# Kernel optimization log

Hardware: AMD Instinct MI355X
Metric: run time of the kernel (lower is better)

## Reference

```python
import jax, jax.numpy as jnp
import numpy as np

B, H, W, DIM = 8, 64, 64, 256
HEADS, DH = 8, 64
HID = HEADS * DH  # 512
EPS = 1e-5


def setup_inputs() -> dict:
    key = jax.random.key(0)
    k0, k1, k2 = jax.random.split(key, 3)
    return {
        "x": jax.random.normal(k0, (B, H, W, DIM), dtype=jnp.float32),
        "w_qkv": jax.random.normal(k1, (DIM, 3 * HID), dtype=jnp.float32) / np.sqrt(DIM),
        "gn_scale": jnp.ones((HID,), jnp.float32),
        "gn_bias": jnp.zeros((HID,), jnp.float32),
        "w_out": jax.random.normal(k2, (HID, DIM), dtype=jnp.float32) / np.sqrt(HID),
        "b_out": jnp.zeros((DIM,), jnp.float32),
    }


def reference(x, w_qkv, gn_scale, gn_bias, w_out, b_out):
    b, h, w, c = x.shape
    n = h * w
    scale = DH ** -0.5
    # 1x1 conv (no bias) == channel matmul
    qkv = jnp.einsum('bxyc,cf->bxyf', x, w_qkv)
    q, k, v = jnp.split(qkv, 3, axis=-1)
    # 'b x y (h c) -> b h c (x y)'
    to_heads = lambda t: t.reshape(b, n, HEADS, DH).transpose(0, 2, 3, 1)
    q, k, v = map(to_heads, (q, k, v))  # [b, heads, d, n]
    q = jax.nn.softmax(q, axis=-2) * scale  # softmax over feature dim d
    k = jax.nn.softmax(k, axis=-1)          # softmax over token dim n
    context = jnp.einsum('bhdn,bhen->bhde', k, v)   # small d x e context
    out = jnp.einsum('bhde,bhdn->bhen', context, q)  # [b, heads, e, n]
    # 'b h c (x y) -> b x y (h c)'
    out = out.transpose(0, 3, 1, 2).reshape(b, h, w, HID)
    # GroupNorm with 1 group: normalize over (H, W, C) per sample
    mu = out.mean(axis=(1, 2, 3), keepdims=True)
    var = out.var(axis=(1, 2, 3), keepdims=True)
    out = (out - mu) * jax.lax.rsqrt(var + EPS) * gn_scale + gn_bias
    # final 1x1 conv with bias
    return jnp.einsum('bxyf,fc->bxyc', out, w_out) + b_out
```

## Files before the change

### kernel.cpp

```cpp
#include <hip/hip_runtime.h>


typedef unsigned short ushort_t;
typedef __attribute__((ext_vector_type(8))) short short8;
typedef __attribute__((ext_vector_type(4))) float floatx4;

__device__ __forceinline__ float b2f(ushort_t u) {
  unsigned int i = ((unsigned int)u) << 16;
  float f;
  __builtin_memcpy(&f, &i, 4);
  return f;
}
__device__ __forceinline__ ushort_t f2b(float f) {
  unsigned int i;
  __builtin_memcpy(&i, &f, 4);
  unsigned int r = (i + 0x7FFFu + ((i >> 16) & 1u)) >> 16;
  return (ushort_t)r;
}

__device__ __forceinline__ void load_lds16(const ushort_t* g, ushort_t* l) {
  __builtin_amdgcn_global_load_lds(
      (const __attribute__((address_space(1))) unsigned int*)g,
      (__attribute__((address_space(3))) unsigned int*)l, 16, 0, 0);
}

__global__ __launch_bounds__(256) void cast_f32_bf16(
    const float* __restrict__ in, ushort_t* __restrict__ out) {
  long i = ((long)blockIdx.x * 256 + threadIdx.x) * 4;
  float4 v = *(const float4*)(in + i);
  ushort4 o;
  o.x = f2b(v.x);
  o.y = f2b(v.y);
  o.z = f2b(v.z);
  o.w = f2b(v.w);
  *(ushort4*)(out + i) = o;
}

__global__ __launch_bounds__(256) void transpose_f32_bf16(
    const float* __restrict__ in, ushort_t* __restrict__ out, int R, int C,
    const float* __restrict__ scale) {
  __shared__ ushort_t t[32][33];
  int c0 = blockIdx.x * 32, r0 = blockIdx.y * 32;
  int tx = threadIdx.x & 31, ty = threadIdx.x >> 5;
  for (int i = 0; i < 32; i += 8) {
    float s = scale ? scale[r0 + ty + i] : 1.0f;
    t[ty + i][tx] = f2b(in[(long)(r0 + ty + i) * C + c0 + tx] * s);
  }
  __syncthreads();
  for (int i = 0; i < 32; i += 8)
    out[(long)(c0 + ty + i) * R + r0 + tx] = t[tx][ty + i];
}

__global__ __launch_bounds__(64) void prep_gw_kernel(
    const float* __restrict__ gn_scale, const float* __restrict__ gn_bias,
    const float* __restrict__ w_out, const float* __restrict__ b_out,
    float* __restrict__ gw1, float* __restrict__ bias2) {
  int c = blockIdx.x * 64 + threadIdx.x;
  float g1 = 0.f, b2 = 0.f;
  for (int f = 0; f < 512; ++f) {
    float w = w_out[f * 256 + c];
    g1 += gn_scale[f] * w;
    b2 += gn_bias[f] * w;
  }
  gw1[c] = g1;
  bias2[c] = b2 + b_out[c];
}

template <int MODE, bool SWAP>
__global__ __launch_bounds__(256) void gemm_tpl(
    const ushort_t* __restrict__ A, const ushort_t* __restrict__ Bt,
    void* __restrict__ Cv, int M, int K, int F,
    const float* __restrict__ murs, const float* __restrict__ gw1,
    const float* __restrict__ bias2) {
  __shared__ __align__(16) ushort_t As[128][32];
  __shared__ __align__(16) ushort_t Bs[128][32];
  int tid = threadIdx.x;
  long m0 = (long)(SWAP ? blockIdx.y : blockIdx.x) * 128;
  long f0 = (long)(SWAP ? blockIdx.x : blockIdx.y) * 128;
  int wv = tid >> 6, lane = tid & 63;
  int wm = wv & 1, wf = wv >> 1;
  int l15 = lane & 15, quad = lane >> 4;

  floatx4 acc[4][4];
  floatx4 zero = {0.f, 0.f, 0.f, 0.f};
  for (int i = 0; i < 4; i++)
    for (int j = 0; j < 4; j++) acc[i][j] = zero;

  for (int k0 = 0; k0 < K; k0 += 32) {
    __syncthreads();
#pragma unroll
    for (int r = 0; r < 2; ++r) {
      int chunk = r * 256 + tid;
      int row = chunk >> 2;
      int kc = chunk & 3;
      load_lds16(A + (m0 + row) * (long)K + k0 + kc * 8, &As[row][kc * 8]);
      load_lds16(Bt + (f0 + row) * (long)K + k0 + kc * 8, &Bs[row][kc * 8]);
    }
    __syncthreads();
    short8 af[4], bfr[4];
#pragma unroll
    for (int mt = 0; mt < 4; mt++)
      af[mt] = *(const short8*)(&As[wm * 64 + mt * 16 + l15][quad * 8]);
#pragma unroll
    for (int ft = 0; ft < 4; ft++)
      bfr[ft] = *(const short8*)(&Bs[wf * 64 + ft * 16 + l15][quad * 8]);
#pragma unroll
    for (int mt = 0; mt < 4; mt++)
#pragma unroll
      for (int ft = 0; ft < 4; ft++)
        acc[mt][ft] = __builtin_amdgcn_mfma_f32_16x16x32_bf16(
            af[mt], bfr[ft], acc[mt][ft], 0, 0, 0);
  }

  {
    float* C = (float*)Cv;
    int b = (int)(m0 >> 12);
    float mu = murs[b * 2], rs = murs[b * 2 + 1];
#pragma unroll
    for (int mt = 0; mt < 4; mt++)
#pragma unroll
      for (int ft = 0; ft < 4; ft++) {
        long col = f0 + wf * 64 + ft * 16 + l15;
        float c1 = bias2[col] - rs * mu * gw1[col];
#pragma unroll
        for (int r = 0; r < 4; r++) {
          long row = m0 + wm * 64 + mt * 16 + quad * 4 + r;
          C[row * F + col] = rs * acc[mt][ft][r] + c1;
        }
      }
  }
}

__global__ __launch_bounds__(256) void kvctx_kernel(
    const ushort_t* __restrict__ xb, const ushort_t* __restrict__ wqkvT,
    float* __restrict__ ctxP, float* __restrict__ ksumP) {
  __shared__ __align__(16) char lds[32768];
  ushort_t* As = (ushort_t*)lds;
  ushort_t* Bs = (ushort_t*)(lds + 16384);
  ushort_t* kTs = (ushort_t*)lds;
  ushort_t* vTs = (ushort_t*)(lds + 16384);

  int gid = blockIdx.x;
  int h = gid >> 7;
  int c0i = gid & 127;
  int b = c0i >> 4;
  int cy = c0i & 15;
  int bh = b * 8 + h;
  int tid = threadIdx.x, wv = tid >> 6, lane = tid & 63;
  int wm = wv & 1, wfk = wv >> 1;
  int l15 = lane & 15, quad = lane >> 4;

  floatx4 zero = {0.f, 0.f, 0.f, 0.f};
  floatx4 cacc[4], acc1;
  for (int i = 0; i < 4; i++) cacc[i] = zero;
  acc1 = zero;
  short8 ones;
#pragma unroll
  for (int u = 0; u < 8; ++u) ones[u] = (short)0x3F80;

  for (int sub = 0; sub < 2; ++sub) {
    long m0 = (long)b * 4096 + cy * 256 + sub * 128;
    floatx4 acc[4][4];
    for (int i = 0; i < 4; i++)
      for (int j = 0; j < 4; j++) acc[i][j] = zero;

    for (int k0 = 0; k0 < 256; k0 += 64) {
      __syncthreads();
#pragma unroll
      for (int r = 0; r < 4; ++r) {
        int chunk = r * 256 + tid;
        int row = chunk >> 3;
        int kc = chunk & 7;
        int gc = kc ^ (row & 7);
        long arow = (row < 64 ? 512 : 960) + h * 64 + row;
        load_lds16(wqkvT + arow * 256 + k0 + gc * 8, As + chunk * 8);
        load_lds16(xb + (m0 + row) * 256 + k0 + gc * 8, Bs + chunk * 8);
      }
      __syncthreads();
#pragma unroll
      for (int ks = 0; ks < 2; ++ks) {
        short8 af[4], bfr[4];
#pragma unroll
        for (int mt = 0; mt < 4; mt++) {
          int row = wfk * 64 + mt * 16 + l15;
          int slot = (ks * 4 + quad) ^ (row & 7);
          af[mt] = *(const short8*)(As + row * 64 + slot * 8);
        }
#pragma unroll
        for (int ft = 0; ft < 4; ft++) {
          int rowb = wm * 64 + ft * 16 + l15;
          int slot = (ks * 4 + quad) ^ (rowb & 7);
          bfr[ft] = *(const short8*)(Bs + rowb * 64 + slot * 8);
        }
#pragma unroll
        for (int mt = 0; mt < 4; mt++)
#pragma unroll
          for (int ft = 0; ft < 4; ft++)
            acc[mt][ft] = __builtin_amdgcn_mfma_f32_16x16x32_bf16(
                af[mt], bfr[ft], acc[mt][ft], 0, 0, 0);
      }
    }
    __syncthreads();

    {
      ushort_t* T = wfk ? vTs : kTs;
#pragma unroll
      for (int mt = 0; mt < 4; mt++)
#pragma unroll
        for (int ft = 0; ft < 4; ft++) {
          int n = wm * 64 + ft * 16 + l15;
          int c = n >> 3, u = n & 7;
#pragma unroll
          for (int r = 0; r < 4; r++) {
            int d = mt * 16 + quad * 4 + r;
            float v = acc[mt][ft][r];
            if (!wfk) v = __expf(v);
            int slot = (c & 8) | ((c ^ d) & 7);
            T[d * 128 + slot * 8 + u] = f2b(v);
          }
        }
    }
    __syncthreads();

#pragma unroll
    for (int ks = 0; ks < 4; ++ks) {
      int d = wv * 16 + l15;
      int cidx = ks * 4 + quad;
      int sa = (cidx & 8) | ((cidx ^ d) & 7);
      short8 a = *(const short8*)(kTs + d * 128 + sa * 8);
      short8 bf[4];
#pragma unroll
      for (int ft = 0; ft < 4; ++ft) {
        int e = ft * 16 + l15;
        int sb = (cidx & 8) | ((cidx ^ e) & 7);
        bf[ft] = *(const short8*)(vTs + e * 128 + sb * 8);
      }
#pragma unroll
      for (int ft = 0; ft < 4; ++ft)
        cacc[ft] = __builtin_amdgcn_mfma_f32_16x16x32_bf16(a, bf[ft], cacc[ft],
                                                           0, 0, 0);
      acc1 = __builtin_amdgcn_mfma_f32_16x16x32_bf16(a, ones, acc1, 0, 0, 0);
    }
  }

  float* cb = ctxP + ((long)cy * 64 + bh) * 4096;
#pragma unroll
  for (int ft = 0; ft < 4; ++ft)
    *(floatx4*)&cb[(ft * 16 + l15) * 64 + wv * 16 + quad * 4] = cacc[ft];
  if (l15 == 0) {
    float* kb = ksumP + ((long)cy * 64 + bh) * 64;
    *(floatx4*)&kb[wv * 16 + quad * 4] = acc1;
  }
}

__global__ __launch_bounds__(256) void reduce_kernel(
    const float* __restrict__ ctxP, const float* __restrict__ ksumP,
    ushort_t* __restrict__ ctxB) {
  int bid = blockIdx.x;
  int bh = bid >> 4;
  int j = (bid & 15) * 256 + threadIdx.x;
  int e = j >> 6, d = j & 63;
  float ks = 0.f;
#pragma unroll
  for (int c = 0; c < 16; ++c) ks += ksumP[((long)c * 64 + bh) * 64 + d];
  float s = 0.f;
#pragma unroll
  for (int c = 0; c < 16; ++c) s += ctxP[((long)c * 64 + bh) * 4096 + j];
  int slot = (d >> 3) ^ (e & 7);
  ctxB[(long)bh * 4096 + e * 64 + slot * 8 + (d & 7)] = f2b(s / ks);
}

__global__ __launch_bounds__(256, 4) void qattn_kernel(
    const ushort_t* __restrict__ xb, const ushort_t* __restrict__ wqT,
    const ushort_t* __restrict__ ctxB, ushort_t* __restrict__ A2,
    float* __restrict__ gstats) {
  __shared__ __align__(16) char lds[32800];
  ushort_t* As = (ushort_t*)lds;
  ushort_t* Bs = (ushort_t*)(lds + 16384);
  ushort_t* P = (ushort_t*)lds;
  ushort_t* Od = (ushort_t*)lds;
  float* red = (float*)(lds + 32768);

  int tid = threadIdx.x;
  int bx = blockIdx.x, by = blockIdx.y;
  long m0 = (long)bx * 128;
  long f0 = (long)by * 128;
  int wv = tid >> 6, lane = tid & 63;
  int wm = wv & 1, wf = wv >> 1;
  int l15 = lane & 15, quad = lane >> 4;
  int b = bx >> 5;

  floatx4 acc[4][4];
  floatx4 zero = {0.f, 0.f, 0.f, 0.f};
  for (int i = 0; i < 4; i++)
    for (int j = 0; j < 4; j++) acc[i][j] = zero;

  for (int k0 = 0; k0 < 256; k0 += 64) {
    __syncthreads();
#pragma unroll
    for (int r = 0; r < 4; ++r) {
      int chunk = r * 256 + tid;
      int row = chunk >> 3;
      int kc = chunk & 7;
      int gc = kc ^ (row & 7);
      load_lds16(xb + (m0 + row) * 256 + k0 + gc * 8, As + chunk * 8);
      load_lds16(wqT + (f0 + row) * 256 + k0 + gc * 8, Bs + chunk * 8);
    }
    __syncthreads();
#pragma unroll
    for (int ks = 0; ks < 2; ++ks) {
      short8 af[4], bfr[4];
#pragma unroll
      for (int mt = 0; mt < 4; mt++) {
        int row = wm * 64 + mt * 16 + l15;
        int slot = (ks * 4 + quad) ^ (row & 7);
        af[mt] = *(const short8*)(As + row * 64 + slot * 8);
      }
#pragma unroll
      for (int ft = 0; ft < 4; ft++) {
        int rowb = wf * 64 + ft * 16 + l15;
        int slot = (ks * 4 + quad) ^ (rowb & 7);
        bfr[ft] = *(const short8*)(Bs + rowb * 64 + slot * 8);
      }
#pragma unroll
      for (int mt = 0; mt < 4; mt++)
#pragma unroll
        for (int ft = 0; ft < 4; ft++)
          acc[mt][ft] = __builtin_amdgcn_mfma_f32_16x16x32_bf16(
              af[mt], bfr[ft], acc[mt][ft], 0, 0, 0);
    }
  }

  const ushort_t* cg = ctxB + ((long)(b * 8 + by * 2 + wf)) * 4096;
  short8 cfr0[4];
#pragma unroll
  for (int ft = 0; ft < 4; ++ft) {
    int e = ft * 16 + l15;
    int slot = quad ^ (e & 7);
    cfr0[ft] = *(const short8*)(cg + e * 64 + slot * 8);
  }

  __syncthreads();

  float rs[4][4];
#pragma unroll
  for (int mt = 0; mt < 4; mt++)
#pragma unroll
    for (int r = 0; r < 4; r++) rs[mt][r] = 0.f;
#pragma unroll
  for (int mt = 0; mt < 4; mt++)
#pragma unroll
    for (int ft = 0; ft < 4; ft++)
#pragma unroll
      for (int r = 0; r < 4; r++) {
        float e = __expf(acc[mt][ft][r]);
        acc[mt][ft][r] = e;
        rs[mt][r] += e;
      }
#pragma unroll
  for (int mt = 0; mt < 4; mt++)
#pragma unroll
    for (int r = 0; r < 4; r++) {
      float t = rs[mt][r];
      t += __shfl_xor(t, 1);
      t += __shfl_xor(t, 2);
      t += __shfl_xor(t, 4);
      t += __shfl_xor(t, 8);
      rs[mt][r] = 0.125f / t;
    }

  {
    ushort_t* Pw = P + wf * 8192;
#pragma unroll
    for (int mt = 0; mt < 4; mt++)
#pragma unroll
      for (int ft = 0; ft < 4; ft++) {
        int d = ft * 16 + l15;
#pragma unroll
        for (int r = 0; r < 4; r++) {
          int row = wm * 64 + mt * 16 + quad * 4 + r;
          int slot = (d >> 3) ^ (row & 7);
          Pw[row * 64 + slot * 8 + (d & 7)] = f2b(acc[mt][ft][r] * rs[mt][r]);
        }
      }
  }

  short8 cfr1[4];
#pragma unroll
  for (int ft = 0; ft < 4; ++ft) {
    int e = ft * 16 + l15;
    int slot = (4 + quad) ^ (e & 7);
    cfr1[ft] = *(const short8*)(cg + e * 64 + slot * 8);
  }

  floatx4 o[4][4];
  for (int i = 0; i < 4; i++)
    for (int j = 0; j < 4; j++) o[i][j] = zero;
  {
    const ushort_t* Pr = P + wf * 8192;
    short8 af[4];
#pragma unroll
    for (int mt = 0; mt < 4; mt++) {
      int row = wm * 64 + mt * 16 + l15;
      int slot = quad ^ (row & 7);
      af[mt] = *(const short8*)(Pr + row * 64 + slot * 8);
    }
#pragma unroll
    for (int mt = 0; mt < 4; mt++)
#pragma unroll
      for (int ft = 0; ft < 4; ft++)
        o[mt][ft] = __builtin_amdgcn_mfma_f32_16x16x32_bf16(af[mt], cfr0[ft],
                                                            o[mt][ft], 0, 0,
                                                            0);
#pragma unroll
    for (int mt = 0; mt < 4; mt++) {
      int row = wm * 64 + mt * 16 + l15;
      int slot = (4 + quad) ^ (row & 7);
      af[mt] = *(const short8*)(Pr + row * 64 + slot * 8);
    }
#pragma unroll
    for (int mt = 0; mt < 4; mt++)
#pragma unroll
      for (int ft = 0; ft < 4; ft++)
        o[mt][ft] = __builtin_amdgcn_mfma_f32_16x16x32_bf16(af[mt], cfr1[ft],
                                                            o[mt][ft], 0, 0,
                                                            0);
  }

  float lsum = 0.f, lss = 0.f;
#pragma unroll
  for (int mt = 0; mt < 4; mt++)
#pragma unroll
    for (int ft = 0; ft < 4; ft++)
#pragma unroll
      for (int r = 0; r < 4; r++) {
        float v = o[mt][ft][r];
        lsum += v;
        lss += v * v;
      }

  __syncthreads();

#pragma unroll
  for (int mt = 0; mt < 4; mt++)
#pragma unroll
    for (int ft = 0; ft < 4; ft++) {
      int cl = wf * 64 + ft * 16 + l15;
      int c = cl >> 3, u = cl & 7;
#pragma unroll
      for (int r = 0; r < 4; r++) {
        int rl = wm * 64 + mt * 16 + quad * 4 + r;
        int slot = (c & 8) | ((c ^ rl) & 7);
        Od[rl * 128 + slot * 8 + u] = f2b(o[mt][ft][r]);
      }
    }
  __syncthreads();

  {
    ushort_t* a2g = A2 + m0 * 512 + f0;
#pragma unroll
    for (int s = 0; s < 8; ++s) {
      int off = s * 2048 + tid * 8;
      int row = off >> 7;
      int c2 = (off & 127) >> 3;
      int slot = (c2 & 8) | ((c2 ^ row) & 7);
      *(short8*)(a2g + (long)row * 512 + c2 * 8) =
          *(const short8*)(Od + row * 128 + slot * 8);
    }
  }

  for (int s = 32; s > 0; s >>= 1) {
    lsum += __shfl_xor(lsum, s);
    lss += __shfl_xor(lss, s);
  }
  if (lane == 0) {
    red[wv * 2] = lsum;
    red[wv * 2 + 1] = lss;
  }
  __syncthreads();
  if (tid == 0) {
    float a = 0.f, c = 0.f;
    for (int w2 = 0; w2 < 4; w2++) {
      a += red[w2 * 2];
      c += red[w2 * 2 + 1];
    }
    atomicAdd(&gstats[b * 2], a);
    atomicAdd(&gstats[b * 2 + 1], c);
  }
}

__global__ __launch_bounds__(64) void finalize_murs(
    const float* __restrict__ gstats, float* __restrict__ murs) {
  int tid = threadIdx.x;
  if (tid < 8) {
    float cnt = 4096.f * 512.f;
    float mu = gstats[tid * 2] / cnt;
    float var = gstats[tid * 2 + 1] / cnt - mu * mu;
    murs[tid * 2] = mu;
    murs[tid * 2 + 1] = rsqrtf(var + 1e-5f);
  }
}

extern "C" void kernel_launch(void* const* d_in, const int* in_sizes, int n_in,
                              void* d_out, int out_size, void* d_ws,
                              size_t ws_size, hipStream_t stream) {
  const float* x = (const float*)d_in[0];
  const float* w_qkv = (const float*)d_in[1];
  const float* gn_scale = (const float*)d_in[2];
  const float* gn_bias = (const float*)d_in[3];
  const float* w_out = (const float*)d_in[4];
  const float* b_out = (const float*)d_in[5];
  float* out = (float*)d_out;

  char* w = (char*)d_ws;
  ushort_t* xb = (ushort_t*)(w + 0);
  ushort_t* A2 = (ushort_t*)(w + 16777216);
  float* ctxP = (float*)(w + 50331648);
  float* ksumP = (float*)(w + 83886080);
  ushort_t* wqkvT = (ushort_t*)(w + 84410368);
  ushort_t* w2T = (ushort_t*)(w + 85196800);
  ushort_t* ctxB = (ushort_t*)(w + 85458944);
  float* gstats = (float*)(w + 85983232);
  float* murs = (float*)(w + 85983296);
  float* bias2 = (float*)(w + 85983360);
  float* gw1 = (float*)(w + 85984384);

  hipMemsetAsync(gstats, 0, 64, stream);

  cast_f32_bf16<<<8388608 / 4 / 256, 256, 0, stream>>>(x, xb);
  transpose_f32_bf16<<<dim3(1536 / 32, 256 / 32), 256, 0, stream>>>(
      w_qkv, wqkvT, 256, 1536, nullptr);
  transpose_f32_bf16<<<dim3(256 / 32, 512 / 32), 256, 0, stream>>>(
      w_out, w2T, 512, 256, gn_scale);
  prep_gw_kernel<<<4, 64, 0, stream>>>(gn_scale, gn_bias, w_out, b_out, gw1,
                                       bias2);
  kvctx_kernel<<<1024, 256, 0, stream>>>(xb, wqkvT, ctxP, ksumP);
  reduce_kernel<<<1024, 256, 0, stream>>>(ctxP, ksumP, ctxB);
  qattn_kernel<<<dim3(256, 4), 256, 0, stream>>>(xb, wqkvT, ctxB, A2, gstats);
  finalize_murs<<<1, 64, 0, stream>>>(gstats, murs);
  gemm_tpl<2, false><<<dim3(256, 2), 256, 0, stream>>>(
      A2, w2T, out, 32768, 512, 256, murs, gw1, bias2);
}
```

Before: 239.5 us.

## Double-buffer GEMM K-loops and split kvctx token chunks across more blocks

The K/V and Q projection GEMM main loops in kvctx_kernel and qattn_kernel now use two LDS buffers with a 32-wide K step, so the next tile's global-to-LDS loads are issued while MFMAs run on the current tile. This replaces the load-then-compute pattern that needed two barriers per step. kvctx_kernel also drops its two-subchunk inner loop and launches 2048 blocks, each covering 128 tokens, with a launch bound of 4 blocks per CU. reduce_kernel now sums 32 partials instead of 16, which doubles partial-buffer traffic and needs ctxP to hold twice as many partials.

```diff
diff --git a/kernel.cpp b/kernel.cpp
--- a/kernel.cpp
+++ b/kernel.cpp
@@ -131,118 +131,118 @@
   }
 }
 
-__global__ __launch_bounds__(256) void kvctx_kernel(
+__global__ __launch_bounds__(256, 4) void kvctx_kernel(
     const ushort_t* __restrict__ xb, const ushort_t* __restrict__ wqkvT,
     float* __restrict__ ctxP, float* __restrict__ ksumP) {
   __shared__ __align__(16) char lds[32768];
-  ushort_t* As = (ushort_t*)lds;
-  ushort_t* Bs = (ushort_t*)(lds + 16384);
   ushort_t* kTs = (ushort_t*)lds;
   ushort_t* vTs = (ushort_t*)(lds + 16384);
 
   int gid = blockIdx.x;
-  int h = gid >> 7;
-  int c0i = gid & 127;
-  int b = c0i >> 4;
-  int cy = c0i & 15;
+  int h = gid >> 8;
+  int c0i = gid & 255;
+  int b = c0i >> 5;
+  int cy = c0i & 31;
   int bh = b * 8 + h;
   int tid = threadIdx.x, wv = tid >> 6, lane = tid & 63;
   int wm = wv & 1, wfk = wv >> 1;
   int l15 = lane & 15, quad = lane >> 4;
+  long m0 = (long)b * 4096 + cy * 128;
 
   floatx4 zero = {0.f, 0.f, 0.f, 0.f};
+  floatx4 acc[4][4];
+  for (int i = 0; i < 4; i++)
+    for (int j = 0; j < 4; j++) acc[i][j] = zero;
+
+  auto stage = [&](int p, int k0) {
+    ushort_t* Ab = (ushort_t*)(lds + p * 16384);
+    ushort_t* Bb = Ab + 4096;
+#pragma unroll
+    for (int r = 0; r < 2; ++r) {
+      int chunk = r * 256 + tid;
+      int row = chunk >> 2, kc = chunk & 3;
+      int gc = kc ^ (row & 3);
+      long arow = (row < 64 ? 512 : 960) + h * 64 + row;
+      load_lds16(wqkvT + arow * 256 + k0 + gc * 8, Ab + chunk * 8);
+      load_lds16(xb + (m0 + row) * 256 + k0 + gc * 8, Bb + chunk * 8);
+    }
+  };
+
+  stage(0, 0);
+  __syncthreads();
+#pragma unroll
+  for (int t = 0; t < 8; ++t) {
+    int p = t & 1;
+    if (t < 7) stage(p ^ 1, (t + 1) * 32);
+    ushort_t* Ab = (ushort_t*)(lds + p * 16384);
+    ushort_t* Bb = Ab + 4096;
+    short8 af[4], bfr[4];
+#pragma unroll
+    for (int mt = 0; mt < 4; mt++) {
+      int row = wfk * 64 + mt * 16 + l15;
+      int slot = quad ^ (row & 3);
+      af[mt] = *(const short8*)(Ab + row * 32 + slot * 8);
+    }
+#pragma unroll
+    for (int ft = 0; ft < 4; ft++) {
+      int rowb = wm * 64 + ft * 16 + l15;
+      int slot = quad ^ (rowb & 3);
+      bfr[ft] = *(const short8*)(Bb + rowb * 32 + slot * 8);
+    }
+#pragma unroll
+    for (int mt = 0; mt < 4; mt++)
+#pragma unroll
+      for (int ft = 0; ft < 4; ft++)
+        acc[mt][ft] = __builtin_amdgcn_mfma_f32_16x16x32_bf16(
+            af[mt], bfr[ft], acc[mt][ft], 0, 0, 0);
+    __syncthreads();
+  }
+
+  {
+    ushort_t* T = wfk ? vTs : kTs;
+#pragma unroll
+    for (int mt = 0; mt < 4; mt++)
+#pragma unroll
+      for (int ft = 0; ft < 4; ft++) {
+        int n = wm * 64 + ft * 16 + l15;
+        int c = n >> 3, u = n & 7;
+#pragma unroll
+        for (int r = 0; r < 4; r++) {
+          int d = mt * 16 + quad * 4 + r;
+          float v = acc[mt][ft][r];
+          if (!wfk) v = __expf(v);
+          int slot = (c & 8) | ((c ^ d) & 7);
+          T[d * 128 + slot * 8 + u] = f2b(v);
+        }
+      }
+  }
+  __syncthreads();
+
   floatx4 cacc[4], acc1;
   for (int i = 0; i < 4; i++) cacc[i] = zero;
   acc1 = zero;
   short8 ones;
 #pragma unroll
   for (int u = 0; u < 8; ++u) ones[u] = (short)0x3F80;
-
-  for (int sub = 0; sub < 2; ++sub) {
-    long m0 = (long)b * 4096 + cy * 256 + sub * 128;
-    floatx4 acc[4][4];
-    for (int i = 0; i < 4; i++)
-      for (int j = 0; j < 4; j++) acc[i][j] = zero;
-
-    for (int k0 = 0; k0 < 256; k0 += 64) {
-      __syncthreads();
-#pragma unroll
-      for (int r = 0; r < 4; ++r) {
-        int chunk = r * 256 + tid;
-        int row = chunk >> 3;
-        int kc = chunk & 7;
-        int gc = kc ^ (row & 7);
-        long arow = (row < 64 ? 512 : 960) + h * 64 + row;
-        load_lds16(wqkvT + arow * 256 + k0 + gc * 8, As + chunk * 8);
-        load_lds16(xb + (m0 + row) * 256 + k0 + gc * 8, Bs + chunk * 8);
-      }
-      __syncthreads();
-#pragma unroll
-      for (int ks = 0; ks < 2; ++ks) {
-        short8 af[4], bfr[4];
-#pragma unroll
-        for (int mt = 0; mt < 4; mt++) {
-          int row = wfk * 64 + mt * 16 + l15;
-          int slot = (ks * 4 + quad) ^ (row & 7);
-          af[mt] = *(const short8*)(As + row * 64 + slot * 8);
-        }
-#pragma unroll
-        for (int ft = 0; ft < 4; ft++) {
-          int rowb = wm * 64 + ft * 16 + l15;
-          int slot = (ks * 4 + quad) ^ (rowb & 7);
-          bfr[ft] = *(const short8*)(Bs + rowb * 64 + slot * 8);
-        }
-#pragma unroll
-        for (int mt = 0; mt < 4; mt++)
-#pragma unroll
-          for (int ft = 0; ft < 4; ft++)
-            acc[mt][ft] = __builtin_amdgcn_mfma_f32_16x16x32_bf16(
-                af[mt], bfr[ft], acc[mt][ft], 0, 0, 0);
-      }
-    }
-    __syncthreads();
-
-    {
-      ushort_t* T = wfk ? vTs : kTs;
-#pragma unroll
-      for (int mt = 0; mt < 4; mt++)
-#pragma unroll
-        for (int ft = 0; ft < 4; ft++) {
-          int n = wm * 64 + ft * 16 + l15;
-          int c = n >> 3, u = n & 7;
-#pragma unroll
-          for (int r = 0; r < 4; r++) {
-            int d = mt * 16 + quad * 4 + r;
-            float v = acc[mt][ft][r];
-            if (!wfk) v = __expf(v);
-            int slot = (c & 8) | ((c ^ d) & 7);
-            T[d * 128 + slot * 8 + u] = f2b(v);
-          }
-        }
-    }
-    __syncthreads();
-
-#pragma unroll
-    for (int ks = 0; ks < 4; ++ks) {
-      int d = wv * 16 + l15;
-      int cidx = ks * 4 + quad;
-      int sa = (cidx & 8) | ((cidx ^ d) & 7);
-      short8 a = *(const short8*)(kTs + d * 128 + sa * 8);
-      short8 bf[4];
-#pragma unroll
-      for (int ft = 0; ft < 4; ++ft) {
-        int e = ft * 16 + l15;
-        int sb = (cidx & 8) | ((cidx ^ e) & 7);
-        bf[ft] = *(const short8*)(vTs + e * 128 + sb * 8);
-      }
-#pragma unroll
-      for (int ft = 0; ft < 4; ++ft)
-        cacc[ft] = __builtin_amdgcn_mfma_f32_16x16x32_bf16(a, bf[ft], cacc[ft],
-                                                           0, 0, 0);
-      acc1 = __builtin_amdgcn_mfma_f32_16x16x32_bf16(a, ones, acc1, 0, 0, 0);
-    }
-  }
-
+#pragma unroll
+  for (int ks = 0; ks < 4; ++ks) {
+    int d = wv * 16 + l15;
+    int cidx = ks * 4 + quad;
+    int sa = (cidx & 8) | ((cidx ^ d) & 7);
+    short8 a = *(const short8*)(kTs + d * 128 + sa * 8);
+    short8 bf[4];
+#pragma unroll
+    for (int ft = 0; ft < 4; ++ft) {
+      int e = ft * 16 + l15;
+      int sb = (cidx & 8) | ((cidx ^ e) & 7);
+      bf[ft] = *(const short8*)(vTs + e * 128 + sb * 8);
+    }
+#pragma unroll
+    for (int ft = 0; ft < 4; ++ft)
+      cacc[ft] = __builtin_amdgcn_mfma_f32_16x16x32_bf16(a, bf[ft], cacc[ft],
+                                                         0, 0, 0);
+    acc1 = __builtin_amdgcn_mfma_f32_16x16x32_bf16(a, ones, acc1, 0, 0, 0);
+  }
   float* cb = ctxP + ((long)cy * 64 + bh) * 4096;
 #pragma unroll
   for (int ft = 0; ft < 4; ++ft)
@@ -262,10 +262,10 @@
   int e = j >> 6, d = j & 63;
   float ks = 0.f;
 #pragma unroll
-  for (int c = 0; c < 16; ++c) ks += ksumP[((long)c * 64 + bh) * 64 + d];
+  for (int c = 0; c < 32; ++c) ks += ksumP[((long)c * 64 + bh) * 64 + d];
   float s = 0.f;
 #pragma unroll
-  for (int c = 0; c < 16; ++c) s += ctxP[((long)c * 64 + bh) * 4096 + j];
+  for (int c = 0; c < 32; ++c) s += ctxP[((long)c * 64 + bh) * 4096 + j];
   int slot = (d >> 3) ^ (e & 7);
   ctxB[(long)bh * 4096 + e * 64 + slot * 8 + (d & 7)] = f2b(s / ks);
 }
@@ -275,8 +275,6 @@
     const ushort_t* __restrict__ ctxB, ushort_t* __restrict__ A2,
     float* __restrict__ gstats) {
   __shared__ __align__(16) char lds[32800];
-  ushort_t* As = (ushort_t*)lds;
-  ushort_t* Bs = (ushort_t*)(lds + 16384);
   ushort_t* P = (ushort_t*)lds;
   ushort_t* Od = (ushort_t*)lds;
   float* red = (float*)(lds + 32768);
@@ -295,40 +293,47 @@
   for (int i = 0; i < 4; i++)
     for (int j = 0; j < 4; j++) acc[i][j] = zero;
 
-  for (int k0 = 0; k0 < 256; k0 += 64) {
+  auto stage = [&](int p, int k0) {
+    ushort_t* Ab = (ushort_t*)(lds + p * 16384);
+    ushort_t* Bb = Ab + 4096;
+#pragma unroll
+    for (int r = 0; r < 2; ++r) {
+      int chunk = r * 256 + tid;
+      int row = chunk >> 2, kc = chunk & 3;
+      int gc = kc ^ (row & 3);
+      load_lds16(xb + (m0 + row) * 256 + k0 + gc * 8, Ab + chunk * 8);
+      load_lds16(wqT + (f0 + row) * 256 + k0 + gc * 8, Bb + chunk * 8);
+    }
+  };
+
+  stage(0, 0);
+  __syncthreads();
+#pragma unroll
+  for (int t = 0; t < 8; ++t) {
+    int p = t & 1;
+    if (t < 7) stage(p ^ 1, (t + 1) * 32);
+    ushort_t* Ab = (ushort_t*)(lds + p * 16384);
+    ushort_t* Bb = Ab + 4096;
+    short8 af[4], bfr[4];
+#pragma unroll
+    for (int mt = 0; mt < 4; mt++) {
+      int row = wm * 64 + mt * 16 + l15;
+      int slot = quad ^ (row & 3);
+      af[mt] = *(const short8*)(Ab + row * 32 + slot * 8);
+    }
+#pragma unroll
+    for (int ft = 0; ft < 4; ft++) {
+      int rowb = wf * 64 + ft * 16 + l15;
+      int slot = quad ^ (rowb & 3);
+      bfr[ft] = *(const short8*)(Bb + rowb * 32 + slot * 8);
+    }
+#pragma unroll
+    for (int mt = 0; mt < 4; mt++)
+#pragma unroll
+      for (int ft = 0; ft < 4; ft++)
+        acc[mt][ft] = __builtin_amdgcn_mfma_f32_16x16x32_bf16(
+            af[mt], bfr[ft], acc[mt][ft], 0, 0, 0);
     __syncthreads();
-#pragma unroll
-    for (int r = 0; r < 4; ++r) {
-      int chunk = r * 256 + tid;
-      int row = chunk >> 3;
-      int kc = chunk & 7;
-      int gc = kc ^ (row & 7);
-      load_lds16(xb + (m0 + row) * 256 + k0 + gc * 8, As + chunk * 8);
-      load_lds16(wqT + (f0 + row) * 256 + k0 + gc * 8, Bs + chunk * 8);
-    }
-    __syncthreads();
-#pragma unroll
-    for (int ks = 0; ks < 2; ++ks) {
-      short8 af[4], bfr[4];
-#pragma unroll
-      for (int mt = 0; mt < 4; mt++) {
-        int row = wm * 64 + mt * 16 + l15;
-        int slot = (ks * 4 + quad) ^ (row & 7);
-        af[mt] = *(const short8*)(As + row * 64 + slot * 8);
-      }
-#pragma unroll
-      for (int ft = 0; ft < 4; ft++) {
-        int rowb = wf * 64 + ft * 16 + l15;
-        int slot = (ks * 4 + quad) ^ (rowb & 7);
-        bfr[ft] = *(const short8*)(Bs + rowb * 64 + slot * 8);
-      }
-#pragma unroll
-      for (int mt = 0; mt < 4; mt++)
-#pragma unroll
-        for (int ft = 0; ft < 4; ft++)
-          acc[mt][ft] = __builtin_amdgcn_mfma_f32_16x16x32_bf16(
-              af[mt], bfr[ft], acc[mt][ft], 0, 0, 0);
-    }
   }
 
   const ushort_t* cg = ctxB + ((long)(b * 8 + by * 2 + wf)) * 4096;
@@ -339,8 +344,6 @@
     int slot = quad ^ (e & 7);
     cfr0[ft] = *(const short8*)(cg + e * 64 + slot * 8);
   }
-
-  __syncthreads();
 
   float rs[4][4];
 #pragma unroll
@@ -534,7 +537,7 @@
       w_out, w2T, 512, 256, gn_scale);
   prep_gw_kernel<<<4, 64, 0, stream>>>(gn_scale, gn_bias, w_out, b_out, gw1,
                                        bias2);
-  kvctx_kernel<<<1024, 256, 0, stream>>>(xb, wqkvT, ctxP, ksumP);
+  kvctx_kernel<<<2048, 256, 0, stream>>>(xb, wqkvT, ctxP, ksumP);
   reduce_kernel<<<1024, 256, 0, stream>>>(ctxP, ksumP, ctxB);
   qattn_kernel<<<dim3(256, 4), 256, 0, stream>>>(xb, wqkvT, ctxB, A2, gstats);
   finalize_murs<<<1, 64, 0, stream>>>(gstats, murs);
```

Measured after the change: 233.4 us. -2.6%, faster.
